# Performance work log

Measured on AMD Instinct MI355X. Metric: run time of the kernel, lower is better.

Reference implementation:

```python
import jax, jax.numpy as jnp
import numpy as np

B, L, D = 256, 1000, 512
V = 670091 + 1          # output_size + 1 dummy/padding row
PAD = V - 1             # padding_idx = output_size


def setup_inputs() -> dict:
    key = jax.random.key(0)
    k1, k2, k3, k4 = jax.random.split(key, 4)
    embed = jax.random.normal(k1, (B, D), dtype=jnp.float32)
    shortlist = jax.random.randint(k2, (B, L), 0, V, dtype=jnp.int64)
    # learned params (kaiming-ish scale); padding row zeroed as in reset_parameters
    weight = (jax.random.normal(k3, (V, D), dtype=jnp.float32) * 0.02).at[PAD].set(0.0)
    bias = (jax.random.normal(k4, (V, 1), dtype=jnp.float32) * 0.02).at[PAD].set(0.0)
    return {"embed": embed, "shortlist": shortlist, "weight": weight, "bias": bias}


def reference(embed, shortlist, weight, bias):
    # F.embedding gather: [B, L, D]
    short_weights = weight[shortlist]
    # matmul(embed.unsqueeze(1), short_weights.permute(0,2,1)).squeeze() -> [B, L]
    out = jnp.einsum('bd,bld->bl', embed, short_weights)
    # short_bias gather [B, L, 1] -> permuted/added -> [B, L]
    out = out + bias[shortlist, 0]
    return out
```

## Files before the change

### kernel.cpp

```cpp
#include <hip/hip_runtime.h>
#include <hip/hip_bf16.h>


#define BB 256
#define LL 1000
#define DD 512
#define LPB 40

__global__ __launch_bounds__(256) void sparse_linear_kernel(
    const float* __restrict__ embed,
    const int*   __restrict__ shortlist,
    const float* __restrict__ weight,
    const float* __restrict__ bias,
    float*       __restrict__ out)
{
    const int b    = blockIdx.y;
    const int lane = threadIdx.x & 63;
    const int wave = threadIdx.x >> 6;

    const float4* e4 = reinterpret_cast<const float4*>(embed + (size_t)b * DD + lane * 8);
    const float4 e0 = e4[0];
    const float4 e1 = e4[1];

    const int l_base = blockIdx.x * LPB;
    const int l_end  = min(LL, l_base + LPB);

    for (int l = l_base + wave; l < l_end; l += 4) {
        const int idx = shortlist[(size_t)b * LL + l];
        const float4* w4 = reinterpret_cast<const float4*>(weight + (size_t)idx * DD + lane * 8);
        const float4 w0 = w4[0];
        const float4 w1 = w4[1];

        float s = e0.x * w0.x + e0.y * w0.y + e0.z * w0.z + e0.w * w0.w
                + e1.x * w1.x + e1.y * w1.y + e1.z * w1.z + e1.w * w1.w;

        #pragma unroll
        for (int off = 32; off > 0; off >>= 1)
            s += __shfl_down(s, off);

        if (lane == 0)
            out[(size_t)b * LL + l] = s + bias[idx];
    }
}

extern "C" void kernel_launch(void* const* d_in, const int* in_sizes, int n_in,
                              void* d_out, int out_size, void* d_ws, size_t ws_size,
                              hipStream_t stream) {
    const float* embed     = (const float*)d_in[0];
    const int*   shortlist = (const int*)  d_in[1];
    const float* weight    = (const float*)d_in[2];
    const float* bias      = (const float*)d_in[3];
    float*       out       = (float*)d_out;

    dim3 grid((LL + LPB - 1) / LPB, BB);
    sparse_linear_kernel<<<grid, 256, 0, stream>>>(embed, shortlist, weight, bias, out);
}
```

Baseline: 100.2 us.

## Split gather into vocabulary-range passes and prefetch shortlist indices per wave

```diff
diff --git a/kernel.cpp b/kernel.cpp
--- a/kernel.cpp
+++ b/kernel.cpp
@@ -5,14 +5,18 @@
 #define BB 256
 #define LL 1000
 #define DD 512
+#define VV 670092
 #define LPB 40
+#define ITERS 10
+#define NPASS 3
 
-__global__ __launch_bounds__(256) void sparse_linear_kernel(
+__global__ __launch_bounds__(256) void sparse_linear_pass(
     const float* __restrict__ embed,
     const int*   __restrict__ shortlist,
     const float* __restrict__ weight,
     const float* __restrict__ bias,
-    float*       __restrict__ out)
+    float*       __restrict__ out,
+    int lo, int hi)
 {
     const int b    = blockIdx.y;
     const int lane = threadIdx.x & 63;
@@ -22,14 +26,25 @@
     const float4 e0 = e4[0];
     const float4 e1 = e4[1];
 
-    const int l_base = blockIdx.x * LPB;
-    const int l_end  = min(LL, l_base + LPB);
+    const int lbase = blockIdx.x * LPB + wave;
 
-    for (int l = l_base + wave; l < l_end; l += 4) {
-        const int idx = shortlist[(size_t)b * LL + l];
-        const float4* w4 = reinterpret_cast<const float4*>(weight + (size_t)idx * DD + lane * 8);
-        const float4 w0 = w4[0];
-        const float4 w1 = w4[1];
+    int pidx = 0;
+    if (lane < ITERS)
+        pidx = shortlist[(size_t)b * LL + lbase + 4 * lane];
+
+    float* orow = out + (size_t)b * LL + lbase;
+
+    #pragma unroll
+    for (int i = 0; i < ITERS; ++i) {
+        const int idx = __shfl(pidx, i);
+        if (idx < lo || idx >= hi) continue;
+
+        float bval = 0.0f;
+        if (lane == 0) bval = bias[idx];
+
+        const float4* wp = reinterpret_cast<const float4*>(weight + (size_t)idx * DD + lane * 8);
+        const float4 w0 = wp[0];
+        const float4 w1 = wp[1];
 
         float s = e0.x * w0.x + e0.y * w0.y + e0.z * w0.z + e0.w * w0.w
                 + e1.x * w1.x + e1.y * w1.y + e1.z * w1.z + e1.w * w1.w;
@@ -39,7 +54,7 @@
             s += __shfl_down(s, off);
 
         if (lane == 0)
-            out[(size_t)b * LL + l] = s + bias[idx];
+            orow[4 * i] = s + bval;
     }
 }
 
@@ -53,5 +68,9 @@
     float*       out       = (float*)d_out;
 
     dim3 grid((LL + LPB - 1) / LPB, BB);
-    sparse_linear_kernel<<<grid, 256, 0, stream>>>(embed, shortlist, weight, bias, out);
+    const int bounds[NPASS + 1] = {0, VV / 3, 2 * (VV / 3), VV};
+    for (int p = 0; p < NPASS; ++p) {
+        sparse_linear_pass<<<grid, 256, 0, stream>>>(
+            embed, shortlist, weight, bias, out, bounds[p], bounds[p + 1]);
+    }
 }
```

After: 100.0 us. No clear change (-0.2%).
